# Performance work log

Measured on AMD Instinct MI355X. Metric: run time of the kernel, lower is better.

Reference implementation:

```python
import math
import jax, jax.numpy as jnp
import numpy as np

B, S, D, H, HD = 2, 2048, 1024, 16, 64  # batch, seq, dim, heads, head_dim
EPS = 1e-5

def setup_inputs() -> dict:
    key = jax.random.key(0)
    ks = jax.random.split(key, 10)
    init = lambda k, shape: jax.random.normal(k, shape, jnp.float32) * 0.02
    return {
        "x": jax.random.normal(ks[0], (B, S, D), jnp.float32),
        "cos": jax.random.uniform(ks[1], (1, S, 1, 1, HD), dtype=jnp.float32),
        "sin": jax.random.uniform(ks[2], (1, S, 1, 1, HD), dtype=jnp.float32),
        "c": jax.random.normal(ks[3], (B, D), jnp.float32),
        "norm1_w": jnp.ones((D,), jnp.float32),
        "w_qkv": init(ks[4], (3 * D, D)),
        "w_out": init(ks[5], (D, D)),
        "norm2_w": jnp.ones((D,), jnp.float32),
        "mlp_w1": init(ks[6], (4 * D, D)),
        "mlp_b1": jnp.zeros((4 * D,), jnp.float32),
        "mlp_w2": init(ks[7], (D, 4 * D)),
        "mlp_b2": jnp.zeros((D,), jnp.float32),
        "ada_w": init(ks[8], (6 * D, D)),
        "ada_b": init(ks[9], (6 * D,)),
    }

def _ln(x, w):
    # LayerNorm computed in fp32, no bias, then scaled by weight
    xf = x.astype(jnp.float32)
    mu = xf.mean(-1, keepdims=True)
    var = xf.var(-1, keepdims=True)
    return (xf - mu) * jax.lax.rsqrt(var + EPS) * w

def _modulate(h, shift, scale):
    return h * (1.0 + scale[:, None, :]) + shift[:, None, :]

def reference(x, cos, sin, c, norm1_w, w_qkv, w_out, norm2_w,
              mlp_w1, mlp_b1, mlp_w2, mlp_b2, ada_w, ada_b):
    # adaLN modulation params: [B, 6D] -> six [B, D] chunks
    ada = c @ ada_w.T + ada_b
    sh_msa, sc_msa, g_msa, sh_mlp, sc_mlp, g_mlp = jnp.split(ada, 6, axis=-1)

    # attention branch (flash_attn path: no rotary applied, naive full softmax)
    h = _modulate(_ln(x, norm1_w), sh_msa, sc_msa)
    qkv = (h @ w_qkv.T).reshape(B, S, 3, H, HD)
    q, k, v = qkv[:, :, 0], qkv[:, :, 1], qkv[:, :, 2]
    scores = jnp.einsum('bqhd,bkhd->bhqk', q, k) / math.sqrt(HD)
    probs = jax.nn.softmax(scores, axis=-1)
    attn = jnp.einsum('bhqk,bkhd->bqhd', probs, v).reshape(B, S, D)
    # gate * dropout(out) + residual; eval mode -> dropout = identity
    x = x + g_msa[:, None, :] * (attn @ w_out.T)

    # MLP branch
    h = _modulate(_ln(x, norm2_w), sh_mlp, sc_mlp)
    h = jax.nn.gelu(h @ mlp_w1.T + mlp_b1, approximate=True) @ mlp_w2.T + mlp_b2
    return x + g_mlp[:, None, :] * h
```

## Files before the change

### kernel.cpp

```cpp
#include <hip/hip_runtime.h>
#include <stdint.h>

typedef __attribute__((ext_vector_type(4))) float f32x4;
typedef __attribute__((ext_vector_type(8))) __bf16 bf16x8;

#define DEV static __device__ __forceinline__

DEV unsigned short f2bf(float f){
    uint32_t u = __float_as_uint(f);
    u += 0x7FFFu + ((u >> 16) & 1u);
    return (unsigned short)(u >> 16);
}
DEV float bf2f(unsigned short s){
    uint32_t u = ((uint32_t)s) << 16;
    return __uint_as_float(u);
}

typedef __attribute__((address_space(1))) const void as1v;
typedef __attribute__((address_space(3))) void as3v;
DEV void g2l16(const void* g, void* l){
    __builtin_amdgcn_global_load_lds((as1v*)g, (as3v*)l, 16, 0, 0);
}

__global__ __launch_bounds__(256) void k_cast_bf16(const float* __restrict__ in,
                                                   unsigned short* __restrict__ out, int n4){
    int i = blockIdx.x * 256 + threadIdx.x;
    if (i < n4){
        float4 v = ((const float4*)in)[i];
        ((ushort4*)out)[i] = make_ushort4(f2bf(v.x), f2bf(v.y), f2bf(v.z), f2bf(v.w));
    }
}

__global__ __launch_bounds__(256) void k_cast_bf16q(const float* __restrict__ in,
                                                    unsigned short* __restrict__ out,
                                                    int n4, int nq4){
    int i = blockIdx.x * 256 + threadIdx.x;
    if (i < n4){
        float4 v = ((const float4*)in)[i];
        float s = (i < nq4) ? 0.18033688011112043f : 1.f;
        ((ushort4*)out)[i] = make_ushort4(f2bf(v.x * s), f2bf(v.y * s), f2bf(v.z * s), f2bf(v.w * s));
    }
}

__global__ __launch_bounds__(256) void k_ada(const float* __restrict__ c,
                                             const float* __restrict__ aw,
                                             const float* __restrict__ ab,
                                             float* __restrict__ out){
    int wid  = blockIdx.x * 4 + (threadIdx.x >> 6);
    int lane = threadIdx.x & 63;
    int b = wid / 6144, r = wid % 6144;
    const float4* cw = (const float4*)(c + (size_t)b * 1024);
    const float4* wr = (const float4*)(aw + (size_t)r * 1024);
    float s = 0.f;
    #pragma unroll
    for (int i = 0; i < 4; i++){
        float4 a = wr[lane + i * 64];
        float4 q = cw[lane + i * 64];
        s += a.x*q.x + a.y*q.y + a.z*q.z + a.w*q.w;
    }
    #pragma unroll
    for (int off = 32; off > 0; off >>= 1) s += __shfl_down(s, off);
    if (lane == 0) out[wid] = s + ab[r];
}

__global__ __launch_bounds__(256) void k_ln_mod(const float* __restrict__ x,
                                                const float* __restrict__ w,
                                                const float* __restrict__ ada,
                                                int sh_off, int sc_off,
                                                unsigned short* __restrict__ out){
    int row = blockIdx.x;
    int b   = row >> 11;
    int tid = threadIdx.x;
    float4 v = ((const float4*)(x + (size_t)row * 1024))[tid];
    float s  = v.x + v.y + v.z + v.w;
    float ss = v.x*v.x + v.y*v.y + v.z*v.z + v.w*v.w;
    #pragma unroll
    for (int off = 32; off > 0; off >>= 1){ s += __shfl_down(s, off); ss += __shfl_down(ss, off); }
    __shared__ float red[8];
    int wv = tid >> 6;
    if ((tid & 63) == 0){ red[wv] = s; red[4 + wv] = ss; }
    __syncthreads();
    float S  = red[0] + red[1] + red[2] + red[3];
    float SS = red[4] + red[5] + red[6] + red[7];
    float mu   = S * (1.f / 1024.f);
    float rstd = rsqrtf(SS * (1.f / 1024.f) - mu * mu + 1e-5f);
    const float* adab = ada + (size_t)b * 6144;
    float4 wv4 = ((const float4*)w)[tid];
    float4 sh  = ((const float4*)(adab + sh_off))[tid];
    float4 sc  = ((const float4*)(adab + sc_off))[tid];
    float h0 = (v.x - mu) * rstd * wv4.x * (1.f + sc.x) + sh.x;
    float h1 = (v.y - mu) * rstd * wv4.y * (1.f + sc.y) + sh.y;
    float h2 = (v.z - mu) * rstd * wv4.z * (1.f + sc.z) + sh.z;
    float h3 = (v.w - mu) * rstd * wv4.w * (1.f + sc.w) + sh.w;
    ((ushort4*)(out + (size_t)row * 1024))[tid] = make_ushort4(f2bf(h0), f2bf(h1), f2bf(h2), f2bf(h3));
}

template<int MODE>
__global__ __launch_bounds__(256, 2) void k_gemm2(const unsigned short* __restrict__ A,
                                                  const unsigned short* __restrict__ B,
                                                  void* __restrict__ outp,
                                                  const float* __restrict__ bias,
                                                  const float* __restrict__ res,
                                                  const float* __restrict__ ada, int goff,
                                                  int M, int N, int K){
    __shared__ unsigned short S[2 * 12288];
    int tid = threadIdx.x, lane = tid & 63, wv = tid >> 6;
    int quad = lane >> 4, l15 = lane & 15;
    int wm = wv & 1, wn = wv >> 1;
    int bm = blockIdx.x, bn = blockIdx.y;
    int klo, khi;
    if constexpr (MODE == 3){
        klo = blockIdx.z * 1376;
        khi = klo + 1376; if (khi > K) khi = K;
    } else {
        klo = 0; khi = K;
    }
    f32x4 acc[8][4] = {};
    int srow = lane >> 2, sseg = lane & 3;
    const unsigned short* ga = A + (size_t)(bm * 256 + wv * 64 + srow) * K + sseg * 8;
    const unsigned short* gb = B + (size_t)(bn * 128 + wv * 32 + srow) * K + sseg * 8;
    size_t k16 = (size_t)16 * K;
    auto STAGE = [&](int buf, int k0){
        unsigned short* as = S + buf * 12288 + wv * 2048;
        unsigned short* bs = S + buf * 12288 + 8192 + wv * 1024;
        g2l16(ga + k0,            as);
        g2l16(ga + k16 + k0,      as + 512);
        g2l16(ga + 2 * k16 + k0,  as + 1024);
        g2l16(ga + 3 * k16 + k0,  as + 1536);
        g2l16(gb + k0,            bs);
        g2l16(gb + k16 + k0,      bs + 512);
    };
    STAGE(0, klo);
    for (int k0 = klo; k0 < khi; k0 += 32){
        int cur = ((k0 - klo) >> 5) & 1;
        __syncthreads();
        if (k0 + 32 < khi) STAGE(cur ^ 1, k0 + 32);
        const unsigned short* as = S + cur * 12288;
        const unsigned short* bs = S + cur * 12288 + 8192;
        bf16x8 af[8], bf[4];
        #pragma unroll
        for (int i = 0; i < 8; i++)
            af[i] = *(const bf16x8*)(as + (wm * 128 + i * 16 + l15) * 32 + quad * 8);
        #pragma unroll
        for (int j = 0; j < 4; j++)
            bf[j] = *(const bf16x8*)(bs + (wn * 64 + j * 16 + l15) * 32 + quad * 8);
        #pragma unroll
        for (int i = 0; i < 8; i++)
            #pragma unroll
            for (int j = 0; j < 4; j++)
                acc[i][j] = __builtin_amdgcn_mfma_f32_16x16x32_bf16(af[i], bf[j], acc[i][j], 0, 0, 0);
    }
    unsigned short* zp = nullptr;
    if constexpr (MODE == 3){
        int z = blockIdx.z;
        if (z < 2) zp = (unsigned short*)outp + (size_t)z * 4194304;
        else       zp = (unsigned short*)(void*)bias;
    }
    int row0 = bm * 256 + wm * 128, col0 = bn * 128 + wn * 64;
    #pragma unroll
    for (int i = 0; i < 8; i++){
        #pragma unroll
        for (int r = 0; r < 4; r++){
            int row = row0 + i * 16 + quad * 4 + r;
            #pragma unroll
            for (int j = 0; j < 4; j++){
                int col = col0 + j * 16 + l15;
                float v = acc[i][j][r];
                size_t idx = (size_t)row * N + col;
                if constexpr (MODE == 0){
                    ((unsigned short*)outp)[idx] = f2bf(v);
                } else if constexpr (MODE == 1){
                    float t = v + bias[col];
                    float u = 1.5957691216057308f * (t + 0.044715f * t * t * t);
                    float g = t / (1.f + __expf(-u));
                    ((unsigned short*)outp)[idx] = f2bf(g);
                } else {
                    zp[idx] = f2bf(v);
                }
            }
        }
    }
}

template<int MODE>
__global__ __launch_bounds__(256) void k_gemm(const unsigned short* __restrict__ A,
                                              const unsigned short* __restrict__ B,
                                              void* __restrict__ outp,
                                              const float* __restrict__ bias,
                                              const float* __restrict__ res,
                                              const float* __restrict__ ada, int goff,
                                              int M, int N, int K){
    __shared__ unsigned short As[3 * 4096];
    __shared__ unsigned short Bs[3 * 4096];
    int tid = threadIdx.x, lane = tid & 63, wv = tid >> 6;
    int quad = lane >> 4, l15 = lane & 15;
    int wm = wv & 1, wn = wv >> 1;
    int bm = blockIdx.x, bn = blockIdx.y;
    int klo = 0, khi = K;
    f32x4 acc[4][4] = {};
    int srow = wv * 16 + (lane >> 2), sseg = lane & 3;
    const unsigned short* ga = A + (size_t)(bm * 128 + srow) * K + sseg * 8;
    const unsigned short* gb = B + (size_t)(bn * 128 + srow) * K + sseg * 8;
    size_t stride64 = (size_t)64 * K;
    int wb = wv * 512;
    int nt = (khi - klo) >> 5;
    auto STAGE = [&](int t, int bufi){
        unsigned short* as = As + bufi * 4096;
        unsigned short* bs = Bs + bufi * 4096;
        int ko = klo + (t << 5);
        g2l16(ga + ko,            as + wb);
        g2l16(ga + stride64 + ko, as + 2048 + wb);
        g2l16(gb + ko,            bs + wb);
        g2l16(gb + stride64 + ko, bs + 2048 + wb);
    };
    STAGE(0, 0);
    STAGE(1, 1);
    for (int t = 0; t < nt; ++t){
        int bi = t % 3;
        if (t){
            __builtin_amdgcn_s_barrier();
            __builtin_amdgcn_sched_barrier(0);
        }
        if (t + 2 < nt) STAGE(t + 2, (t + 2) % 3);
        if (t + 2 < nt)      asm volatile("s_waitcnt vmcnt(8)" ::: "memory");
        else if (t + 1 < nt) asm volatile("s_waitcnt vmcnt(4)" ::: "memory");
        else                 asm volatile("s_waitcnt vmcnt(0)" ::: "memory");
        __builtin_amdgcn_s_barrier();
        __builtin_amdgcn_sched_barrier(0);
        const unsigned short* as = As + bi * 4096;
        const unsigned short* bs = Bs + bi * 4096;
        bf16x8 af[4], bfr[4];
        #pragma unroll
        for (int i = 0; i < 4; i++)
            af[i] = *(const bf16x8*)(as + (wm * 64 + i * 16 + l15) * 32 + quad * 8);
        #pragma unroll
        for (int j = 0; j < 4; j++)
            bfr[j] = *(const bf16x8*)(bs + (wn * 64 + j * 16 + l15) * 32 + quad * 8);
        #pragma unroll
        for (int i = 0; i < 4; i++)
            #pragma unroll
            for (int j = 0; j < 4; j++)
                acc[i][j] = __builtin_amdgcn_mfma_f32_16x16x32_bf16(af[i], bfr[j], acc[i][j], 0, 0, 0);
    }
    int row0 = bm * 128 + wm * 64, col0 = bn * 128 + wn * 64;
    #pragma unroll
    for (int i = 0; i < 4; i++){
        #pragma unroll
        for (int r = 0; r < 4; r++){
            int row = row0 + i * 16 + quad * 4 + r;
            #pragma unroll
            for (int j = 0; j < 4; j++){
                int col = col0 + j * 16 + l15;
                float v = acc[i][j][r];
                size_t idx = (size_t)row * N + col;
                if constexpr (MODE == 2){
                    float t2 = v;
                    if (bias) t2 += bias[col];
                    int bb = row >> 11;
                    float g = ada[(size_t)bb * 6144 + goff + col];
                    ((float*)outp)[idx] = res[idx] + g * t2;
                } else {
                    ((unsigned short*)outp)[idx] = f2bf(v);
                }
            }
        }
    }
}

__global__ __launch_bounds__(256) void k_ep2(const unsigned short* __restrict__ z01,
                                             const unsigned short* __restrict__ z2,
                                             const float* __restrict__ bias,
                                             const float* __restrict__ res,
                                             const float* __restrict__ ada, int goff,
                                             float* __restrict__ out){
    int row = blockIdx.x;
    int bb  = row >> 11;
    int tid = threadIdx.x;
    size_t base = (size_t)row * 1024 + tid * 4;
    ushort4 a0 = *(const ushort4*)(z01 + base);
    ushort4 a1 = *(const ushort4*)(z01 + 4194304 + base);
    ushort4 a2 = *(const ushort4*)(z2 + base);
    float4 rv = *(const float4*)(res + base);
    float4 bv = ((const float4*)bias)[tid];
    float4 gv = ((const float4*)(ada + (size_t)bb * 6144 + goff))[tid];
    float4 o;
    o.x = rv.x + gv.x * (bf2f(a0.x) + bf2f(a1.x) + bf2f(a2.x) + bv.x);
    o.y = rv.y + gv.y * (bf2f(a0.y) + bf2f(a1.y) + bf2f(a2.y) + bv.y);
    o.z = rv.z + gv.z * (bf2f(a0.z) + bf2f(a1.z) + bf2f(a2.z) + bv.z);
    o.w = rv.w + gv.w * (bf2f(a0.w) + bf2f(a1.w) + bf2f(a2.w) + bv.w);
    *(float4*)(out + base) = o;
}

__global__ __launch_bounds__(256) void k_vt(const unsigned short* __restrict__ qkv,
                                            unsigned short* __restrict__ vt){
    __shared__ unsigned short T[64 * 66];
    int kb = blockIdx.x, bh = blockIdx.y;
    int b = bh >> 4, h = bh & 15;
    size_t rb = (size_t)b * 2048;
    int t = threadIdx.x;
    int key = t >> 2, seg = t & 3;
    const unsigned short* src = qkv + (rb + kb * 64 + key) * 3072 + 2048 + h * 64;
    uint4 v0 = *(const uint4*)(src + seg * 8);
    uint4 v1 = *(const uint4*)(src + 32 + seg * 8);
    const unsigned short* p0 = (const unsigned short*)&v0;
    const unsigned short* p1 = (const unsigned short*)&v1;
    unsigned short* tr = T + key * 66;
    ushort2* t0 = (ushort2*)(tr + seg * 8);
    ushort2* t1 = (ushort2*)(tr + 32 + seg * 8);
    #pragma unroll
    for (int j = 0; j < 4; j++){
        t0[j] = make_ushort2(p0[2*j], p0[2*j+1]);
        t1[j] = make_ushort2(p1[2*j], p1[2*j+1]);
    }
    __syncthreads();
    int d = t >> 2, kseg = t & 3;
    unsigned short obuf[16];
    #pragma unroll
    for (int j = 0; j < 16; j++) obuf[j] = T[(kseg * 16 + j) * 66 + d];
    uint4* dst = (uint4*)(vt + ((size_t)bh * 64 + d) * 2048 + kb * 64 + kseg * 16);
    dst[0] = ((const uint4*)obuf)[0];
    dst[1] = ((const uint4*)obuf)[1];
}

__global__ __launch_bounds__(256) void k_attn(const unsigned short* __restrict__ qkv,
                                              const unsigned short* __restrict__ vt,
                                              unsigned short* __restrict__ out){
    __shared__ unsigned short Ks[2 * 4096];
    __shared__ unsigned short Vs[2 * 4096];
    __shared__ __align__(16) unsigned short Ps[4 * 32 * 72];
    int tid = threadIdx.x, lane = tid & 63, wv = tid >> 6;
    int quad = lane >> 4, l15 = lane & 15;
    int qt = blockIdx.x, bh = blockIdx.y;
    int b = bh >> 4, h = bh & 15;
    size_t rb = (size_t)b * 2048;

    bf16x8 qb[2][2];
    #pragma unroll
    for (int t = 0; t < 2; t++){
        int qrow = qt * 128 + wv * 32 + t * 16 + l15;
        const unsigned short* qp = qkv + ((rb + qrow) * 3072 + h * 64 + quad * 8);
        qb[t][0] = *(const bf16x8*)qp;
        qb[t][1] = *(const bf16x8*)(qp + 32);
    }
    bf16x8 ONES;
    #pragma unroll
    for (int i = 0; i < 8; i++) ONES[i] = (__bf16)1.0f;
    f32x4 ls[2] = {};
    f32x4 o[2][4];
    #pragma unroll
    for (int t = 0; t < 2; t++)
        #pragma unroll
        for (int dt = 0; dt < 4; dt++) o[t][dt] = (f32x4){0.f, 0.f, 0.f, 0.f};

    int rr = wv * 16 + (lane >> 2), cs = lane & 3;
    const unsigned short* gk = qkv + (rb + rr) * 3072 + 1024 + h * 64 + cs * 8;
    const unsigned short* gv = vt + ((size_t)bh * 64 + rr) * 2048 + cs * 8;
    int soff = rr * 32 + (cs ^ ((rr >> 1) & 3)) * 8;
    int rsl = (quad ^ ((l15 >> 1) & 3)) * 8;
    unsigned short* Pw = Ps + wv * 32 * 72;

    uint4 rk0 = *(const uint4*)(gk);
    uint4 rk1 = *(const uint4*)(gk + 32);
    uint4 rv0 = *(const uint4*)(gv);
    uint4 rv1 = *(const uint4*)(gv + 32);

    for (int k0 = 0; k0 < 2048; k0 += 64){
        unsigned short* ks = Ks + ((k0 >> 6) & 1) * 4096;
        unsigned short* vs = Vs + ((k0 >> 6) & 1) * 4096;
        int kn = (k0 + 64 < 2048) ? (k0 + 64) : k0;
        uint4 nk0 = *(const uint4*)(gk + (size_t)kn * 3072);
        uint4 nk1 = *(const uint4*)(gk + (size_t)kn * 3072 + 32);
        uint4 nv0 = *(const uint4*)(gv + kn);
        uint4 nv1 = *(const uint4*)(gv + kn + 32);
        *(uint4*)(ks + soff)        = rk0;
        *(uint4*)(ks + 2048 + soff) = rk1;
        *(uint4*)(vs + soff)        = rv0;
        *(uint4*)(vs + 2048 + soff) = rv1;
        __syncthreads();
        rk0 = nk0; rk1 = nk1; rv0 = nv0; rv1 = nv1;
        f32x4 c[2][4];
        #pragma unroll
        for (int kt = 0; kt < 4; kt++){
            bf16x8 ka0 = *(const bf16x8*)(ks + (kt * 16 + l15) * 32 + rsl);
            bf16x8 ka1 = *(const bf16x8*)(ks + 2048 + (kt * 16 + l15) * 32 + rsl);
            #pragma unroll
            for (int t = 0; t < 2; t++){
                f32x4 z = (f32x4){0.f, 0.f, 0.f, 0.f};
                z = __builtin_amdgcn_mfma_f32_16x16x32_bf16(ka0, qb[t][0], z, 0, 0, 0);
                z = __builtin_amdgcn_mfma_f32_16x16x32_bf16(ka1, qb[t][1], z, 0, 0, 0);
                c[t][kt] = z;
            }
        }
        #pragma unroll
        for (int t = 0; t < 2; t++){
            #pragma unroll
            for (int kt = 0; kt < 4; kt++){
                float p0 = __builtin_amdgcn_exp2f(c[t][kt][0]);
                float p1 = __builtin_amdgcn_exp2f(c[t][kt][1]);
                float p2 = __builtin_amdgcn_exp2f(c[t][kt][2]);
                float p3 = __builtin_amdgcn_exp2f(c[t][kt][3]);
                union { uint2 u; __bf16 bh4[4]; } w;
                w.bh4[0] = (__bf16)p0;
                w.bh4[1] = (__bf16)p1;
                w.bh4[2] = (__bf16)p2;
                w.bh4[3] = (__bf16)p3;
                *(uint2*)(Pw + (t * 16 + l15) * 72 + kt * 16 + quad * 4) = w.u;
            }
        }
        bf16x8 pa[2][2];
        #pragma unroll
        for (int t = 0; t < 2; t++){
            pa[t][0] = *(const bf16x8*)(Pw + (t * 16 + l15) * 72 + quad * 8);
            pa[t][1] = *(const bf16x8*)(Pw + (t * 16 + l15) * 72 + 32 + quad * 8);
        }
        #pragma unroll
        for (int t = 0; t < 2; t++){
            ls[t] = __builtin_amdgcn_mfma_f32_16x16x32_bf16(pa[t][0], ONES, ls[t], 0, 0, 0);
            ls[t] = __builtin_amdgcn_mfma_f32_16x16x32_bf16(pa[t][1], ONES, ls[t], 0, 0, 0);
        }
        #pragma unroll
        for (int dt = 0; dt < 4; dt++){
            bf16x8 vb0 = *(const bf16x8*)(vs + (dt * 16 + l15) * 32 + rsl);
            bf16x8 vb1 = *(const bf16x8*)(vs + 2048 + (dt * 16 + l15) * 32 + rsl);
            #pragma unroll
            for (int t = 0; t < 2; t++){
                o[t][dt] = __builtin_amdgcn_mfma_f32_16x16x32_bf16(pa[t][0], vb0, o[t][dt], 0, 0, 0);
                o[t][dt] = __builtin_amdgcn_mfma_f32_16x16x32_bf16(pa[t][1], vb1, o[t][dt], 0, 0, 0);
            }
        }
    }
    #pragma unroll
    for (int t = 0; t < 2; t++){
        #pragma unroll
        for (int r = 0; r < 4; r++){
            float inv = 1.f / ls[t][r];
            int row = qt * 128 + wv * 32 + t * 16 + quad * 4 + r;
            unsigned short* op = out + ((rb + row) * 1024 + h * 64);
            #pragma unroll
            for (int dt = 0; dt < 4; dt++)
                op[dt * 16 + l15] = f2bf(o[t][dt][r] * inv);
        }
    }
}

extern "C" void kernel_launch(void* const* d_in, const int* in_sizes, int n_in,
                              void* d_out, int out_size, void* d_ws, size_t ws_size,
                              hipStream_t stream){
    const float* x     = (const float*)d_in[0];
    const float* c     = (const float*)d_in[3];
    const float* n1w   = (const float*)d_in[4];
    const float* w_qkv = (const float*)d_in[5];
    const float* w_out = (const float*)d_in[6];
    const float* n2w   = (const float*)d_in[7];
    const float* w1    = (const float*)d_in[8];
    const float* b1    = (const float*)d_in[9];
    const float* w2    = (const float*)d_in[10];
    const float* b2    = (const float*)d_in[11];
    const float* ada_w = (const float*)d_in[12];
    const float* ada_b = (const float*)d_in[13];
    float* out = (float*)d_out;
    char* ws = (char*)d_ws;

    unsigned short* wqkv_b = (unsigned short*)(ws + 0);
    unsigned short* wout_b = (unsigned short*)(ws + 6291456);
    unsigned short* w1_b   = (unsigned short*)(ws + 8388608);
    unsigned short* w2_b   = (unsigned short*)(ws + 16777216);
    float*          ada    = (float*)         (ws + 25165824);
    unsigned short* h      = (unsigned short*)(ws + 25214976);
    unsigned short* qkv    = (unsigned short*)(ws + 33603584);
    unsigned short* attn   = (unsigned short*)(ws + 58769408);
    float*          xn     = (float*)         (ws + 67158016);
    unsigned short* u      = qkv;
    unsigned short* vt     = h;
    unsigned short* z01 = (unsigned short*)(ws + 0);
    unsigned short* z2  = (unsigned short*)(ws + 25214976);

    k_cast_bf16q<<<3072, 256, 0, stream>>>(w_qkv, wqkv_b, 786432, 262144);
    k_cast_bf16<<<1024, 256, 0, stream>>>(w_out, wout_b,  262144);
    k_cast_bf16<<<4096, 256, 0, stream>>>(w1,    w1_b,   1048576);
    k_cast_bf16<<<4096, 256, 0, stream>>>(w2,    w2_b,   1048576);
    k_ada<<<3072, 256, 0, stream>>>(c, ada_w, ada_b, ada);
    k_ln_mod<<<4096, 256, 0, stream>>>(x, n1w, ada, 0, 1024, h);
    k_gemm2<0><<<dim3(16, 24), 256, 0, stream>>>(h, wqkv_b, qkv, nullptr, nullptr, nullptr, 0, 4096, 3072, 1024);
    k_vt<<<dim3(32, 32), 256, 0, stream>>>(qkv, vt);
    k_attn<<<dim3(16, 32), 256, 0, stream>>>(qkv, vt, attn);
    k_gemm<2><<<dim3(32, 8), 256, 0, stream>>>(attn, wout_b, xn, nullptr, x, ada, 2048, 4096, 1024, 1024);
    k_ln_mod<<<4096, 256, 0, stream>>>(xn, n2w, ada, 3072, 4096, h);
    k_gemm2<1><<<dim3(16, 32), 256, 0, stream>>>(h, w1_b, u, b1, nullptr, nullptr, 0, 4096, 4096, 1024);
    k_gemm2<3><<<dim3(16, 8, 3), 256, 0, stream>>>(u, w2_b, z01, (const float*)z2, nullptr,
                                                   nullptr, 0, 4096, 1024, 4096);
    k_ep2<<<4096, 256, 0, stream>>>(z01, z2, b2, xn, ada, 5120, out);
}
```

Baseline: 390.2 us.

## Split attention over two key halves and combine partial results

Adds a third grid dimension to the attention kernel so each block handles only half of the 2048 keys. This doubles the number of blocks to give the GPU more parallel work. Each block writes its unnormalized bf16 output and its row sums to workspace, and a new combine kernel adds the two halves and normalizes. In exchange it costs an extra launch, extra global traffic for the partial outputs, and some precision because unnormalized partials are rounded to bf16. The combine is only exact because the softmax uses no per-half running max.

```diff
diff --git a/kernel.cpp b/kernel.cpp
--- a/kernel.cpp
+++ b/kernel.cpp
@@ -324,15 +324,17 @@
 
 __global__ __launch_bounds__(256) void k_attn(const unsigned short* __restrict__ qkv,
                                               const unsigned short* __restrict__ vt,
-                                              unsigned short* __restrict__ out){
+                                              unsigned short* __restrict__ oh,
+                                              float* __restrict__ lsb){
     __shared__ unsigned short Ks[2 * 4096];
     __shared__ unsigned short Vs[2 * 4096];
     __shared__ __align__(16) unsigned short Ps[4 * 32 * 72];
     int tid = threadIdx.x, lane = tid & 63, wv = tid >> 6;
     int quad = lane >> 4, l15 = lane & 15;
-    int qt = blockIdx.x, bh = blockIdx.y;
+    int qt = blockIdx.x, bh = blockIdx.y, kvh = blockIdx.z;
     int b = bh >> 4, h = bh & 15;
     size_t rb = (size_t)b * 2048;
+    int klo2 = kvh << 10, kend = klo2 + 1024;
 
     bf16x8 qb[2][2];
     #pragma unroll
@@ -359,15 +361,15 @@
     int rsl = (quad ^ ((l15 >> 1) & 3)) * 8;
     unsigned short* Pw = Ps + wv * 32 * 72;
 
-    uint4 rk0 = *(const uint4*)(gk);
-    uint4 rk1 = *(const uint4*)(gk + 32);
-    uint4 rv0 = *(const uint4*)(gv);
-    uint4 rv1 = *(const uint4*)(gv + 32);
-
-    for (int k0 = 0; k0 < 2048; k0 += 64){
+    uint4 rk0 = *(const uint4*)(gk + (size_t)klo2 * 3072);
+    uint4 rk1 = *(const uint4*)(gk + (size_t)klo2 * 3072 + 32);
+    uint4 rv0 = *(const uint4*)(gv + klo2);
+    uint4 rv1 = *(const uint4*)(gv + klo2 + 32);
+
+    for (int k0 = klo2; k0 < kend; k0 += 64){
         unsigned short* ks = Ks + ((k0 >> 6) & 1) * 4096;
         unsigned short* vs = Vs + ((k0 >> 6) & 1) * 4096;
-        int kn = (k0 + 64 < 2048) ? (k0 + 64) : k0;
+        int kn = (k0 + 64 < kend) ? (k0 + 64) : k0;
         uint4 nk0 = *(const uint4*)(gk + (size_t)kn * 3072);
         uint4 nk1 = *(const uint4*)(gk + (size_t)kn * 3072 + 32);
         uint4 nv0 = *(const uint4*)(gv + kn);
@@ -429,18 +431,40 @@
             }
         }
     }
+    unsigned short* ohh = oh + (size_t)kvh * 4194304;
+    float* lsh = lsb + (size_t)kvh * 65536;
     #pragma unroll
     for (int t = 0; t < 2; t++){
         #pragma unroll
         for (int r = 0; r < 4; r++){
-            float inv = 1.f / ls[t][r];
             int row = qt * 128 + wv * 32 + t * 16 + quad * 4 + r;
-            unsigned short* op = out + ((rb + row) * 1024 + h * 64);
+            size_t grow = rb + row;
+            unsigned short* op = ohh + (grow * 1024 + h * 64);
             #pragma unroll
             for (int dt = 0; dt < 4; dt++)
-                op[dt * 16 + l15] = f2bf(o[t][dt][r] * inv);
-        }
-    }
+                op[dt * 16 + l15] = f2bf(o[t][dt][r]);
+            if (l15 == 0) lsh[grow * 16 + h] = ls[t][r];
+        }
+    }
+}
+
+__global__ __launch_bounds__(256) void k_cmb(const unsigned short* __restrict__ oh,
+                                             const float* __restrict__ lsb,
+                                             unsigned short* __restrict__ out){
+    int row = blockIdx.x;
+    int tid = threadIdx.x;
+    int col = tid * 4;
+    int h = col >> 6;
+    size_t base = (size_t)row * 1024 + col;
+    ushort4 a = *(const ushort4*)(oh + base);
+    ushort4 b = *(const ushort4*)(oh + 4194304 + base);
+    float inv = 1.f / (lsb[row * 16 + h] + lsb[65536 + row * 16 + h]);
+    ushort4 o;
+    o.x = f2bf((bf2f(a.x) + bf2f(b.x)) * inv);
+    o.y = f2bf((bf2f(a.y) + bf2f(b.y)) * inv);
+    o.z = f2bf((bf2f(a.z) + bf2f(b.z)) * inv);
+    o.w = f2bf((bf2f(a.w) + bf2f(b.w)) * inv);
+    *(ushort4*)(out + base) = o;
 }
 
 extern "C" void kernel_launch(void* const* d_in, const int* in_sizes, int n_in,
@@ -472,6 +496,8 @@
     float*          xn     = (float*)         (ws + 67158016);
     unsigned short* u      = qkv;
     unsigned short* vt     = h;
+    unsigned short* oh  = (unsigned short*)(ws + 67158016);
+    float*          lsb = (float*)         (ws + 0);
     unsigned short* z01 = (unsigned short*)(ws + 0);
     unsigned short* z2  = (unsigned short*)(ws + 25214976);
 
@@ -483,7 +509,8 @@
     k_ln_mod<<<4096, 256, 0, stream>>>(x, n1w, ada, 0, 1024, h);
     k_gemm2<0><<<dim3(16, 24), 256, 0, stream>>>(h, wqkv_b, qkv, nullptr, nullptr, nullptr, 0, 4096, 3072, 1024);
     k_vt<<<dim3(32, 32), 256, 0, stream>>>(qkv, vt);
-    k_attn<<<dim3(16, 32), 256, 0, stream>>>(qkv, vt, attn);
+    k_attn<<<dim3(16, 32, 2), 256, 0, stream>>>(qkv, vt, oh, lsb);
+    k_cmb<<<4096, 256, 0, stream>>>(oh, lsb, attn);
     k_gemm<2><<<dim3(32, 8), 256, 0, stream>>>(attn, wout_b, xn, nullptr, x, ada, 2048, 4096, 1024, 1024);
     k_ln_mod<<<4096, 256, 0, stream>>>(xn, n2w, ada, 3072, 4096, h);
     k_gemm2<1><<<dim3(16, 32), 256, 0, stream>>>(h, w1_b, u, b1, nullptr, nullptr, 0, 4096, 4096, 1024);
```

Result: no change. 392.3 us (+0.5%).
